# Performance work log

Hardware: AMD Instinct MI355X
Metric: run time of the kernel (lower is better)

The kernel has to match this reference:

```python
import jax, jax.numpy as jnp
import numpy as np

ALPHA = 0.1

def grad_f(p):
    # analytic gradient of f(p) = sum(p**2)
    return 2.0 * p

def setup_inputs() -> dict:
    key = jax.random.key(0)
    p = jax.random.normal(key, (16384, 64), dtype=jnp.float32)
    return {"p": p}

def reference(p):
    # p: [N, D]
    g = grad_f(p)                                   # [N, D]
    scores = jnp.einsum('id,jd->ij', g, g)          # torch.inner(g, g) -> [N, N]
    w = jax.nn.softmax(-scores, axis=-1)            # [N, N]
    # einsum('ijd,ij->id', p[None,:,:]-p[:,None,:], w)
    #   = w @ p - sum_j(w[i,j]) * p[i]   (avoids the NxNxD intermediate)
    agg = jnp.matmul(w, p) - jnp.sum(w, axis=-1, keepdims=True) * p  # [N, D]
    return p + agg * ALPHA
```

## Files before the change

kernel.cpp:

```cpp
#include <hip/hip_runtime.h>
#include <stdint.h>

#define NROWS 16384
#define DIM 64
#define BK 64
#define NT (NROWS / BK)
#define NQT (NROWS / 64)
#define TILE_BYTES 16384
#define VT_OFF 8192
#define LOG2E 1.4426950408889634f
#define MHAT_COEF 20.0f

typedef __attribute__((ext_vector_type(8))) _Float16 f16x8;
typedef __attribute__((ext_vector_type(8))) unsigned short ushort8;
typedef __attribute__((ext_vector_type(4))) float f32x4;
typedef __attribute__((ext_vector_type(8))) __bf16 bf16x8;
typedef __attribute__((ext_vector_type(8))) short short8;

static __device__ __forceinline__ f32x4 mfma_f16(f16x8 a, f16x8 b, f32x4 c) {
  return __builtin_amdgcn_mfma_f32_16x16x32_f16(a, b, c, 0, 0, 0);
}
static __device__ __forceinline__ f32x4 mfma_bf16(short8 a, short8 b, f32x4 c) {
  return __builtin_amdgcn_mfma_f32_16x16x32_bf16(
      __builtin_bit_cast(bf16x8, a), __builtin_bit_cast(bf16x8, b), c, 0, 0, 0);
}
static __device__ __forceinline__ void gload_lds16(const void* g, void* l) {
  __builtin_amdgcn_global_load_lds(
      (const __attribute__((address_space(1))) unsigned int*)(uintptr_t)g,
      (__attribute__((address_space(3))) unsigned int*)(unsigned int)(uintptr_t)l,
      16, 0, 0);
}
static __device__ __forceinline__ float fast_exp2(float x) {
  return __builtin_amdgcn_exp2f(x);
}
static __device__ __forceinline__ unsigned short f2bfbits(float x) {
  return __builtin_bit_cast(unsigned short, (__bf16)x);
}
static __device__ __forceinline__ unsigned short f2bf(float x) {
  unsigned u = __builtin_bit_cast(unsigned, x);
  u = (u + 0x7fffu + ((u >> 16) & 1u)) >> 16;
  return (unsigned short)u;
}
static __device__ __forceinline__ float bf2f(unsigned short b) {
  return __builtin_bit_cast(float, ((unsigned)b) << 16);
}

__global__ __launch_bounds__(256)
void pack_kernel(const float* __restrict__ p, unsigned char* __restrict__ tiles,
                 float* __restrict__ mhat) {
  __shared__ unsigned short sT[64][68];
  const int kt = blockIdx.x;
  const int t  = threadIdx.x;
  const int r  = t >> 2;
  const int q4 = t & 3;
  const int d0 = q4 * 16;

  const float* src = p + ((size_t)(kt * 64 + r)) * DIM + d0;
  float4 f0 = ((const float4*)src)[0];
  float4 f1 = ((const float4*)src)[1];
  float4 f2 = ((const float4*)src)[2];
  float4 f3 = ((const float4*)src)[3];
  float v[16] = {f0.x, f0.y, f0.z, f0.w, f1.x, f1.y, f1.z, f1.w,
                 f2.x, f2.y, f2.z, f2.w, f3.x, f3.y, f3.z, f3.w};
  ushort8 h0, h1, hb0, hb1;
  float sq = 0.f;
#pragma unroll
  for (int i = 0; i < 8; ++i) {
    h0[i]  = __builtin_bit_cast(unsigned short, (_Float16)v[i]);
    h1[i]  = __builtin_bit_cast(unsigned short, (_Float16)v[8 + i]);
    hb0[i] = f2bf(v[i]);
    hb1[i] = f2bf(v[8 + i]);
    sq = fmaf(v[i], v[i], sq);
    sq = fmaf(v[8 + i], v[8 + i], sq);
  }
  unsigned char* tb = tiles + (size_t)kt * TILE_BYTES;
  const int swz = (r & 7) << 4;
  *(ushort8*)(tb + r * 128 + ((2 * d0) ^ swz))      = h0;
  *(ushort8*)(tb + r * 128 + ((2 * d0 + 16) ^ swz)) = h1;

  sq += __shfl_xor(sq, 1);
  sq += __shfl_xor(sq, 2);
  if (q4 == 0) mhat[kt * 64 + r] = MHAT_COEF * LOG2E * sqrtf(sq);

  *(ushort8*)&sT[r][d0]     = hb0;
  *(ushort8*)&sT[r][d0 + 8] = hb1;
  __syncthreads();
  const int d    = t >> 2;
  const int base = (q4 >> 1) * 32 + (q4 & 1) * 8;
  ushort8 a8, b8;
#pragma unroll
  for (int j = 0; j < 8; ++j) {
    a8[j] = sT[base + (j >> 2) * 16 + (j & 3)][d];
    b8[j] = sT[base + (j >> 2) * 16 + 4 + (j & 3)][d];
  }
  const int swzd = (d & 7) << 4;
  *(ushort8*)(tb + VT_OFF + d * 128 + ((2 * (q4 * 16)) ^ swzd))      = a8;
  *(ushort8*)(tb + VT_OFF + d * 128 + ((2 * (q4 * 16) + 16) ^ swzd)) = b8;
}

__global__ __launch_bounds__(256)
void attn_main(const float* __restrict__ p, const unsigned char* __restrict__ tiles,
               const float* __restrict__ mhat, float* __restrict__ out,
               float* __restrict__ partO, float* __restrict__ partL,
               int S, int writeDirect) {
  __shared__ __align__(16) unsigned char sbuf[2][TILE_BYTES];

  const int t  = threadIdx.x;
  const int w  = t >> 6;
  const int l  = t & 63;
  const int lr = l & 15;
  const int lg = l >> 4;
  const int qt = blockIdx.x;
  const int s  = blockIdx.y;
  const int ntp = NT / S;
  const int kt0 = s * ntp;
  const int swz = (lr & 7) << 4;
  const int ko0 = (lg * 16) ^ swz;
  const int ko1 = (64 + lg * 16) ^ swz;

  const unsigned char* qtb = tiles + (size_t)qt * TILE_BYTES;
  f16x8 qf[2];
  qf[0] = *(const f16x8*)(qtb + (w * 16 + lr) * 128 + ko0);
  qf[1] = *(const f16x8*)(qtb + (w * 16 + lr) * 128 + ko1);
  const float nm = -mhat[qt * 64 + w * 16 + lr];

  const f32x4 z4 = {0.f, 0.f, 0.f, 0.f};
  f32x4 oacc[4] = {z4, z4, z4, z4};
  float lrun = 0.f;
  const float S2 = -4.0f * LOG2E;

  auto STAGE = [&](int kt, int b) {
    const unsigned char* g = tiles + (size_t)kt * TILE_BYTES + (w * 4) * 1024 + l * 16;
    unsigned char* lb = &sbuf[b][(w * 4) * 1024];
#pragma unroll
    for (int c = 0; c < 4; ++c)
      gload_lds16(g + c * 1024, lb + c * 1024);
  };

  STAGE(kt0, 0);
  __syncthreads();

  for (int i = 0; i < ntp; ++i) {
    if (i + 1 < ntp) STAGE(kt0 + i + 1, (i + 1) & 1);

    const unsigned char* kb = &sbuf[i & 1][0];

    f32x4 acc[4] = {z4, z4, z4, z4};
#pragma unroll
    for (int c = 0; c < 4; ++c) {
      f16x8 kf0 = *(const f16x8*)(kb + (c * 16 + lr) * 128 + ko0);
      f16x8 kf1 = *(const f16x8*)(kb + (c * 16 + lr) * 128 + ko1);
      acc[c] = mfma_f16(kf0, qf[0], acc[c]);
      acc[c] = mfma_f16(kf1, qf[1], acc[c]);
    }

    float pe[4][4];
#pragma unroll
    for (int c = 0; c < 4; ++c) {
#pragma unroll
      for (int r = 0; r < 4; ++r)
        pe[c][r] = fast_exp2(fmaf(acc[c][r], S2, nm));
      lrun += (pe[c][0] + pe[c][1]) + (pe[c][2] + pe[c][3]);
    }
    short8 pb0, pb1;
#pragma unroll
    for (int r = 0; r < 4; ++r) {
      pb0[r]     = (short)f2bfbits(pe[0][r]);
      pb0[4 + r] = (short)f2bfbits(pe[1][r]);
      pb1[r]     = (short)f2bfbits(pe[2][r]);
      pb1[4 + r] = (short)f2bfbits(pe[3][r]);
    }

#pragma unroll
    for (int kc = 0; kc < 2; ++kc) {
      const int ko = kc ? ko1 : ko0;
      const short8 pa = kc ? pb1 : pb0;
#pragma unroll
      for (int dc = 0; dc < 4; ++dc) {
        short8 vb = *(const short8*)(kb + VT_OFF + (dc * 16 + lr) * 128 + ko);
        oacc[dc] = mfma_bf16(pa, vb, oacc[dc]);
      }
    }

    __syncthreads();
  }

  float lsum = lrun;
  lsum += __shfl_xor(lsum, 16);
  lsum += __shfl_xor(lsum, 32);

  if (writeDirect) {
    float lq[4];
#pragma unroll
    for (int r = 0; r < 4; ++r) lq[r] = __shfl(lsum, lg * 4 + r);
#pragma unroll
    for (int r = 0; r < 4; ++r) {
      const float inv = 1.0f / lq[r];
      const size_t grow = (size_t)(qt * 64 + w * 16 + lg * 4 + r) * DIM;
#pragma unroll
      for (int dc = 0; dc < 4; ++dc) {
        const int col = dc * 16 + lr;
        const float pv = p[grow + col];
        out[grow + col] = pv + 0.1f * (oacc[dc][r] * inv - pv);
      }
    }
  } else {
    float* po = partO + (size_t)(qt * S + s) * 4096;
    float* pl = partL + (size_t)(qt * S + s) * 64;
#pragma unroll
    for (int r = 0; r < 4; ++r) {
      const int row = w * 16 + lg * 4 + r;
#pragma unroll
      for (int dc = 0; dc < 4; ++dc)
        po[row * 64 + dc * 16 + lr] = oacc[dc][r];
    }
    if (l < 16) pl[w * 16 + l] = lsum;
  }
}

__global__ __launch_bounds__(256)
void reduce_kernel(const float* __restrict__ p, const float* __restrict__ partO,
                   const float* __restrict__ partL, float* __restrict__ out, int S) {
  const int t   = threadIdx.x;
  const int row = blockIdx.x * 16 + (t >> 4);
  const int c0  = (t & 15) * 4;
  const int qt  = row >> 6;
  const int rin = row & 63;

  float L = 0.f;
  float4 O = {0.f, 0.f, 0.f, 0.f};
  for (int s2 = 0; s2 < S; ++s2) {
    const size_t b = (size_t)(qt * S + s2);
    L += partL[b * 64 + rin];
    const float4 o4 = *(const float4*)&partO[b * 4096 + rin * 64 + c0];
    O.x += o4.x; O.y += o4.y; O.z += o4.z; O.w += o4.w;
  }
  const float inv = 1.0f / L;
  const float4 pv = *(const float4*)&p[(size_t)row * DIM + c0];
  float4 r;
  r.x = pv.x + 0.1f * (O.x * inv - pv.x);
  r.y = pv.y + 0.1f * (O.y * inv - pv.y);
  r.z = pv.z + 0.1f * (O.z * inv - pv.z);
  r.w = pv.w + 0.1f * (O.w * inv - pv.w);
  *(float4*)&out[(size_t)row * DIM + c0] = r;
}

#define LDE 88
__global__ __launch_bounds__(256)
void grad_attn_fb(const float* __restrict__ p, float* __restrict__ out) {
  __shared__ __align__(16) unsigned short sKhi[BK][LDE];
  __shared__ __align__(16) unsigned short sKlo[BK][LDE];
  __shared__ __align__(16) unsigned short sVt[DIM][LDE];
  __shared__ __align__(16) unsigned short sP[4][16][LDE];
  const int t = threadIdx.x, w = t >> 6, l = t & 63, lr = l & 15, lg = l >> 4;
  const int q0 = blockIdx.x * 64 + w * 16;
  short8 qhi[2], qlo[2];
#pragma unroll
  for (int kc = 0; kc < 2; ++kc) {
    const float* qp = p + (size_t)(q0 + lr) * DIM + kc * 32 + lg * 8;
    float4 fa = *(const float4*)qp;
    float4 fb = *(const float4*)(qp + 4);
    float v[8] = {fa.x, fa.y, fa.z, fa.w, fb.x, fb.y, fb.z, fb.w};
    short8 h, lo2;
#pragma unroll
    for (int i = 0; i < 8; ++i) {
      unsigned short hb = f2bf(v[i]);
      h[i] = (short)hb;
      lo2[i] = (short)f2bf(v[i] - bf2f(hb));
    }
    qhi[kc] = h; qlo[kc] = lo2;
  }
  const f32x4 z4 = {0.f, 0.f, 0.f, 0.f};
  f32x4 oacc[4] = {z4, z4, z4, z4};
  float mrun[4] = {-1e30f, -1e30f, -1e30f, -1e30f};
  float lrun[4] = {0.f, 0.f, 0.f, 0.f};
  const int srow = (t >> 3) * 2, sc0 = (t & 7) * 8;
  const int scs = sc0 ^ (((srow >> 3) & 7) << 3);
  const float S2 = -4.0f * LOG2E;
  for (int kt = 0; kt < NT; ++kt) {
    const int kv0 = kt * BK;
    __syncthreads();
    {
      const float* s0 = p + (size_t)(kv0 + srow) * DIM + sc0;
      float4 a0 = *(const float4*)s0;
      float4 b0 = *(const float4*)(s0 + 4);
      float4 a1 = *(const float4*)(s0 + DIM);
      float4 b1 = *(const float4*)(s0 + DIM + 4);
      float v0[8] = {a0.x, a0.y, a0.z, a0.w, b0.x, b0.y, b0.z, b0.w};
      float v1[8] = {a1.x, a1.y, a1.z, a1.w, b1.x, b1.y, b1.z, b1.w};
      short8 h0, h1, l0, l1;
#pragma unroll
      for (int i = 0; i < 8; ++i) {
        unsigned short hb0 = f2bf(v0[i]);
        unsigned short hb1 = f2bf(v1[i]);
        h0[i] = (short)hb0; l0[i] = (short)f2bf(v0[i] - bf2f(hb0));
        h1[i] = (short)hb1; l1[i] = (short)f2bf(v1[i] - bf2f(hb1));
      }
      *(short8*)&sKhi[srow][scs] = h0;
      *(short8*)&sKlo[srow][scs] = l0;
      *(short8*)&sKhi[srow + 1][scs] = h1;
      *(short8*)&sKlo[srow + 1][scs] = l1;
#pragma unroll
      for (int i = 0; i < 8; ++i) {
        int d = sc0 + i;
        unsigned pk = (unsigned)(unsigned short)h0[i] |
                      (((unsigned)(unsigned short)h1[i]) << 16);
        *(unsigned*)&sVt[d][srow ^ (((d >> 3) & 7) << 3)] = pk;
      }
    }
    __syncthreads();
    f32x4 acc[4] = {z4, z4, z4, z4};
#pragma unroll
    for (int c = 0; c < 4; ++c) {
      const int krow = c * 16 + lr;
      const int swc = ((krow >> 3) & 7) << 3;
#pragma unroll
      for (int kc = 0; kc < 2; ++kc) {
        const int off = (kc * 32 + lg * 8) ^ swc;
        short8 bh = *(const short8*)&sKhi[krow][off];
        short8 bl = *(const short8*)&sKlo[krow][off];
        acc[c] = mfma_bf16(qhi[kc], bh, acc[c]);
        acc[c] = mfma_bf16(qhi[kc], bl, acc[c]);
        acc[c] = mfma_bf16(qlo[kc], bh, acc[c]);
      }
    }
    float P[4][4];
#pragma unroll
    for (int r = 0; r < 4; ++r) {
      float e0 = acc[0][r] * S2, e1 = acc[1][r] * S2;
      float e2 = acc[2][r] * S2, e3 = acc[3][r] * S2;
      float mt = fmaxf(fmaxf(e0, e1), fmaxf(e2, e3));
      mt = fmaxf(mt, __shfl_xor(mt, 1));
      mt = fmaxf(mt, __shfl_xor(mt, 2));
      mt = fmaxf(mt, __shfl_xor(mt, 4));
      mt = fmaxf(mt, __shfl_xor(mt, 8));
      const float mn = fmaxf(mrun[r], mt);
      const float sc = exp2f(mrun[r] - mn);
      mrun[r] = mn;
      float p0 = exp2f(e0 - mn), p1 = exp2f(e1 - mn);
      float p2 = exp2f(e2 - mn), p3 = exp2f(e3 - mn);
      P[0][r] = p0; P[1][r] = p1; P[2][r] = p2; P[3][r] = p3;
      float ps = (p0 + p1) + (p2 + p3);
      ps += __shfl_xor(ps, 1);
      ps += __shfl_xor(ps, 2);
      ps += __shfl_xor(ps, 4);
      ps += __shfl_xor(ps, 8);
      lrun[r] = lrun[r] * sc + ps;
#pragma unroll
      for (int dc = 0; dc < 4; ++dc) oacc[dc][r] *= sc;
    }
    {
      const int irow = lg * 4;
      const int swp = ((l >> 5) & 1) << 3;
#pragma unroll
      for (int c = 0; c < 4; ++c) {
        const int colb = (c * 16 + lr) ^ swp;
#pragma unroll
        for (int r = 0; r < 4; ++r) sP[w][irow + r][colb] = f2bf(P[c][r]);
      }
    }
#pragma unroll
    for (int kc = 0; kc < 2; ++kc) {
      const int kb = kc * 32 + lg * 8;
      short8 pa = *(const short8*)&sP[w][lr][kb ^ (((lr >> 3) & 1) << 3)];
#pragma unroll
      for (int dc = 0; dc < 4; ++dc) {
        const int d = dc * 16 + lr;
        short8 vb = *(const short8*)&sVt[d][kb ^ (((d >> 3) & 7) << 3)];
        oacc[dc] = mfma_bf16(pa, vb, oacc[dc]);
      }
    }
  }
#pragma unroll
  for (int r = 0; r < 4; ++r) {
    const float inv = 1.0f / lrun[r];
    const size_t grow = (size_t)(q0 + lg * 4 + r) * DIM;
#pragma unroll
    for (int dc = 0; dc < 4; ++dc) {
      const int col = dc * 16 + lr;
      const float pv = p[grow + col];
      out[grow + col] = pv + 0.1f * (oacc[dc][r] * inv - pv);
    }
  }
}

extern "C" void kernel_launch(void* const* d_in, const int* in_sizes, int n_in,
                              void* d_out, int out_size, void* d_ws, size_t ws_size,
                              hipStream_t stream) {
  const float* p = (const float*)d_in[0];
  float* out = (float*)d_out;
  unsigned char* ws = (unsigned char*)d_ws;
  const size_t tiles_bytes = (size_t)NT * TILE_BYTES;
  const size_t mhat_bytes  = (size_t)NROWS * sizeof(float);
  const size_t base = tiles_bytes + mhat_bytes;

  if (ws_size < base) {
    grad_attn_fb<<<dim3(NQT), dim3(256), 0, stream>>>(p, out);
    return;
  }
  int S = 8;
  while (S > 1) {
    size_t need = base + (size_t)NQT * S * (4096 + 64) * sizeof(float);
    if (need <= ws_size) break;
    S >>= 1;
  }
  float* mhat  = (float*)(ws + tiles_bytes);
  float* partO = (float*)(ws + base);
  float* partL = partO + (size_t)NQT * S * 4096;

  pack_kernel<<<dim3(NT), dim3(256), 0, stream>>>(p, ws, mhat);
  attn_main<<<dim3(NQT, S), dim3(256), 0, stream>>>(p, ws, mhat, out, partO, partL,
                                                    S, S == 1 ? 1 : 0);
  if (S > 1)
    reduce_kernel<<<dim3(NROWS / 16), dim3(256), 0, stream>>>(p, partO, partL, out, S);
}
```

Before: 102.5 us.

## Process 128 query rows per block to reuse each staged key tile twice

Each wave now handles two 16-row query groups instead of one, so a block covers 128 queries and every key/value tile staged in LDS feeds twice as many MFMAs. This halves the number of query blocks and the global/LDS traffic per unit of work. The split-K factor is raised from 8 to 16 to keep the grid size unchanged, and the partial buffers and reduce indexing are resized to match. The cost is roughly double the accumulator registers per thread, which may lower occupancy.

```diff
diff --git a/kernel.cpp b/kernel.cpp
--- a/kernel.cpp
+++ b/kernel.cpp
@@ -5,7 +5,7 @@
 #define DIM 64
 #define BK 64
 #define NT (NROWS / BK)
-#define NQT (NROWS / 64)
+#define NQB (NROWS / 128)
 #define TILE_BYTES 16384
 #define VT_OFF 8192
 #define LOG2E 1.4426950408889634f
@@ -118,15 +118,22 @@
   const int ko0 = (lg * 16) ^ swz;
   const int ko1 = (64 + lg * 16) ^ swz;
 
-  const unsigned char* qtb = tiles + (size_t)qt * TILE_BYTES;
-  f16x8 qf[2];
-  qf[0] = *(const f16x8*)(qtb + (w * 16 + lr) * 128 + ko0);
-  qf[1] = *(const f16x8*)(qtb + (w * 16 + lr) * 128 + ko1);
-  const float nm = -mhat[qt * 64 + w * 16 + lr];
+  f16x8 qf[2][2];
+  float nm[2];
+#pragma unroll
+  for (int g = 0; g < 2; ++g) {
+    const int grow = w * 32 + g * 16;
+    const unsigned char* qtb =
+        tiles + (size_t)(qt * 2 + (grow >> 6)) * TILE_BYTES;
+    const int rin = (grow & 63) + lr;
+    qf[g][0] = *(const f16x8*)(qtb + rin * 128 + ko0);
+    qf[g][1] = *(const f16x8*)(qtb + rin * 128 + ko1);
+    nm[g] = -mhat[qt * 128 + grow + lr];
+  }
 
   const f32x4 z4 = {0.f, 0.f, 0.f, 0.f};
-  f32x4 oacc[4] = {z4, z4, z4, z4};
-  float lrun = 0.f;
+  f32x4 oacc[2][4] = {{z4, z4, z4, z4}, {z4, z4, z4, z4}};
+  float lrun[2] = {0.f, 0.f};
   const float S2 = -4.0f * LOG2E;
 
   auto STAGE = [&](int kt, int b) {
@@ -145,76 +152,84 @@
 
     const unsigned char* kb = &sbuf[i & 1][0];
 
-    f32x4 acc[4] = {z4, z4, z4, z4};
+    f32x4 acc[2][4] = {{z4, z4, z4, z4}, {z4, z4, z4, z4}};
 #pragma unroll
     for (int c = 0; c < 4; ++c) {
       f16x8 kf0 = *(const f16x8*)(kb + (c * 16 + lr) * 128 + ko0);
       f16x8 kf1 = *(const f16x8*)(kb + (c * 16 + lr) * 128 + ko1);
-      acc[c] = mfma_f16(kf0, qf[0], acc[c]);
-      acc[c] = mfma_f16(kf1, qf[1], acc[c]);
-    }
-
-    float pe[4][4];
-#pragma unroll
-    for (int c = 0; c < 4; ++c) {
-#pragma unroll
-      for (int r = 0; r < 4; ++r)
-        pe[c][r] = fast_exp2(fmaf(acc[c][r], S2, nm));
-      lrun += (pe[c][0] + pe[c][1]) + (pe[c][2] + pe[c][3]);
-    }
-    short8 pb0, pb1;
-#pragma unroll
-    for (int r = 0; r < 4; ++r) {
-      pb0[r]     = (short)f2bfbits(pe[0][r]);
-      pb0[4 + r] = (short)f2bfbits(pe[1][r]);
-      pb1[r]     = (short)f2bfbits(pe[2][r]);
-      pb1[4 + r] = (short)f2bfbits(pe[3][r]);
+      acc[0][c] = mfma_f16(kf0, qf[0][0], acc[0][c]);
+      acc[1][c] = mfma_f16(kf0, qf[1][0], acc[1][c]);
+      acc[0][c] = mfma_f16(kf1, qf[0][1], acc[0][c]);
+      acc[1][c] = mfma_f16(kf1, qf[1][1], acc[1][c]);
+    }
+
+    short8 pb[2][2];
+#pragma unroll
+    for (int g = 0; g < 2; ++g) {
+      float pe[4][4];
+#pragma unroll
+      for (int c = 0; c < 4; ++c) {
+#pragma unroll
+        for (int r = 0; r < 4; ++r)
+          pe[c][r] = fast_exp2(fmaf(acc[g][c][r], S2, nm[g]));
+        lrun[g] += (pe[c][0] + pe[c][1]) + (pe[c][2] + pe[c][3]);
+      }
+#pragma unroll
+      for (int r = 0; r < 4; ++r) {
+        pb[g][0][r]     = (short)f2bfbits(pe[0][r]);
+        pb[g][0][4 + r] = (short)f2bfbits(pe[1][r]);
+        pb[g][1][r]     = (short)f2bfbits(pe[2][r]);
+        pb[g][1][4 + r] = (short)f2bfbits(pe[3][r]);
+      }
     }
 
 #pragma unroll
     for (int kc = 0; kc < 2; ++kc) {
       const int ko = kc ? ko1 : ko0;
-      const short8 pa = kc ? pb1 : pb0;
 #pragma unroll
       for (int dc = 0; dc < 4; ++dc) {
         short8 vb = *(const short8*)(kb + VT_OFF + (dc * 16 + lr) * 128 + ko);
-        oacc[dc] = mfma_bf16(pa, vb, oacc[dc]);
+        oacc[0][dc] = mfma_bf16(pb[0][kc], vb, oacc[0][dc]);
+        oacc[1][dc] = mfma_bf16(pb[1][kc], vb, oacc[1][dc]);
       }
     }
 
     __syncthreads();
   }
 
-  float lsum = lrun;
-  lsum += __shfl_xor(lsum, 16);
-  lsum += __shfl_xor(lsum, 32);
-
-  if (writeDirect) {
-    float lq[4];
-#pragma unroll
-    for (int r = 0; r < 4; ++r) lq[r] = __shfl(lsum, lg * 4 + r);
-#pragma unroll
-    for (int r = 0; r < 4; ++r) {
-      const float inv = 1.0f / lq[r];
-      const size_t grow = (size_t)(qt * 64 + w * 16 + lg * 4 + r) * DIM;
-#pragma unroll
-      for (int dc = 0; dc < 4; ++dc) {
-        const int col = dc * 16 + lr;
-        const float pv = p[grow + col];
-        out[grow + col] = pv + 0.1f * (oacc[dc][r] * inv - pv);
-      }
-    }
-  } else {
-    float* po = partO + (size_t)(qt * S + s) * 4096;
-    float* pl = partL + (size_t)(qt * S + s) * 64;
-#pragma unroll
-    for (int r = 0; r < 4; ++r) {
-      const int row = w * 16 + lg * 4 + r;
-#pragma unroll
-      for (int dc = 0; dc < 4; ++dc)
-        po[row * 64 + dc * 16 + lr] = oacc[dc][r];
-    }
-    if (l < 16) pl[w * 16 + l] = lsum;
+#pragma unroll
+  for (int g = 0; g < 2; ++g) {
+    float lsum = lrun[g];
+    lsum += __shfl_xor(lsum, 16);
+    lsum += __shfl_xor(lsum, 32);
+
+    if (writeDirect) {
+      float lq[4];
+#pragma unroll
+      for (int r = 0; r < 4; ++r) lq[r] = __shfl(lsum, lg * 4 + r);
+#pragma unroll
+      for (int r = 0; r < 4; ++r) {
+        const float inv = 1.0f / lq[r];
+        const size_t grow = (size_t)(qt * 128 + w * 32 + g * 16 + lg * 4 + r) * DIM;
+#pragma unroll
+        for (int dc = 0; dc < 4; ++dc) {
+          const int col = dc * 16 + lr;
+          const float pv = p[grow + col];
+          out[grow + col] = pv + 0.1f * (oacc[g][dc][r] * inv - pv);
+        }
+      }
+    } else {
+      float* po = partO + (size_t)(qt * S + s) * 8192;
+      float* pl = partL + (size_t)(qt * S + s) * 128;
+#pragma unroll
+      for (int r = 0; r < 4; ++r) {
+        const int row = w * 32 + g * 16 + lg * 4 + r;
+#pragma unroll
+        for (int dc = 0; dc < 4; ++dc)
+          po[row * 64 + dc * 16 + lr] = oacc[g][dc][r];
+      }
+      if (l < 16) pl[w * 32 + g * 16 + l] = lsum;
+    }
   }
 }
 
@@ -224,15 +239,15 @@
   const int t   = threadIdx.x;
   const int row = blockIdx.x * 16 + (t >> 4);
   const int c0  = (t & 15) * 4;
-  const int qt  = row >> 6;
-  const int rin = row & 63;
+  const int qt  = row >> 7;
+  const int rin = row & 127;
 
   float L = 0.f;
   float4 O = {0.f, 0.f, 0.f, 0.f};
   for (int s2 = 0; s2 < S; ++s2) {
     const size_t b = (size_t)(qt * S + s2);
-    L += partL[b * 64 + rin];
-    const float4 o4 = *(const float4*)&partO[b * 4096 + rin * 64 + c0];
+    L += partL[b * 128 + rin];
+    const float4 o4 = *(const float4*)&partO[b * 8192 + rin * 64 + c0];
     O.x += o4.x; O.y += o4.y; O.z += o4.z; O.w += o4.w;
   }
   const float inv = 1.0f / L;
@@ -395,21 +410,21 @@
   const size_t base = tiles_bytes + mhat_bytes;
 
   if (ws_size < base) {
-    grad_attn_fb<<<dim3(NQT), dim3(256), 0, stream>>>(p, out);
+    grad_attn_fb<<<dim3(NROWS / 64), dim3(256), 0, stream>>>(p, out);
     return;
   }
-  int S = 8;
+  int S = 16;
   while (S > 1) {
-    size_t need = base + (size_t)NQT * S * (4096 + 64) * sizeof(float);
+    size_t need = base + (size_t)NQB * S * (8192 + 128) * sizeof(float);
     if (need <= ws_size) break;
     S >>= 1;
   }
   float* mhat  = (float*)(ws + tiles_bytes);
   float* partO = (float*)(ws + base);
-  float* partL = partO + (size_t)NQT * S * 4096;
+  float* partL = partO + (size_t)NQB * S * 8192;
 
   pack_kernel<<<dim3(NT), dim3(256), 0, stream>>>(p, ws, mhat);
-  attn_main<<<dim3(NQT, S), dim3(256), 0, stream>>>(p, ws, mhat, out, partO, partL,
+  attn_main<<<dim3(NQB, S), dim3(256), 0, stream>>>(p, ws, mhat, out, partO, partL,
                                                     S, S == 1 ? 1 : 0);
   if (S > 1)
     reduce_kernel<<<dim3(NROWS / 16), dim3(256), 0, stream>>>(p, partO, partL, out, S);
```

Result: faster. 97.40 us (-4.9%).
